# Optimization experiments

Hardware: AMD Instinct MI355X
Metric: run time of the kernel (lower is better)

## Reference

```python
import jax, jax.numpy as jnp
import numpy as np

# ---------- e3nn-style machinery, max_l = 1, real basis ----------
_EPS3 = np.zeros((3, 3, 3), dtype=np.float64)
_EPS3[0, 1, 2] = _EPS3[1, 2, 0] = _EPS3[2, 0, 1] = 1.0
_EPS3[0, 2, 1] = _EPS3[2, 1, 0] = _EPS3[1, 0, 2] = -1.0
W3J = {
    (0, 0, 0): np.ones((1, 1, 1)),
    (0, 1, 1): np.eye(3)[None, :, :] / np.sqrt(3.0),
    (1, 0, 1): np.eye(3)[:, None, :] / np.sqrt(3.0),
    (1, 1, 0): np.eye(3)[:, :, None] / np.sqrt(3.0),
    (1, 1, 1): _EPS3 / np.sqrt(6.0),
}

# irreps as (mul, l, parity)
IR_SH    = [(1, 0, 1), (1, 1, -1)]                      # 1x0e+1x1o (dim 4)
IR_INTER = [(4, 0, 1), (4, 0, -1), (2, 1, -1), (2, 1, 1)]  # gate.irreps_in (dim 20)
IR_GOUT  = [(2, 0, 1), (2, 0, -1), (2, 1, -1), (2, 1, 1)]  # gate.irreps_out (dim 16)
IR_OUT   = [(1, 1, -1), (1, 1, 1)]                      # 1x1o+1x1e (dim 6)

def _offsets(ir):
    off, o = [], 0
    for m, l, _ in ir:
        off.append(o)
        o += m * (2 * l + 1)
    return off, o

def build_tp(ir1, ir2, iro):
    """Fully-connected TP instructions: component irrep-norm, element path-norm."""
    fan = [0.0] * len(iro)
    paths = []
    for io, (mo, lo, po) in enumerate(iro):
        for i1, (m1, l1, p1) in enumerate(ir1):
            for i2, (m2, l2, p2) in enumerate(ir2):
                if p1 * p2 == po and abs(l1 - l2) <= lo <= l1 + l2:
                    paths.append((i1, i2, io))
                    fan[io] += m1 * m2
    ins, woff = [], 0
    for i1, i2, io in paths:
        m1, l1, _ = ir1[i1]; m2, l2, _ = ir2[i2]; mo, lo, _ = iro[io]
        alpha = float(np.sqrt((2 * lo + 1) / fan[io]))
        ins.append((i1, i2, io, alpha, woff))
        woff += m1 * m2 * mo
    return ins, woff

INS1, NUMEL1 = build_tp(IR_SH, IR_SH, IR_INTER)   # weight_numel = 14
INS2, NUMEL2 = build_tp(IR_GOUT, IR_SH, IR_OUT)   # weight_numel = 12

def tp_apply(ir1, ir2, iro, ins, x1, x2, w):
    off1, _ = _offsets(ir1); off2, _ = _offsets(ir2); offo, _ = _offsets(iro)
    lead = x1.shape[:-1]
    out = [None] * len(iro)
    for i1, i2, io, alpha, woff in ins:
        m1, l1, _ = ir1[i1]; m2, l2, _ = ir2[i2]; mo, lo, _ = iro[io]
        x1b = x1[..., off1[i1]:off1[i1] + m1 * (2 * l1 + 1)].reshape(lead + (m1, 2 * l1 + 1))
        x2b = x2[..., off2[i2]:off2[i2] + m2 * (2 * l2 + 1)].reshape(lead + (m2, 2 * l2 + 1))
        wb = w[..., woff:woff + m1 * m2 * mo].reshape(lead + (m1, m2, mo))
        C = jnp.asarray(W3J[(l1, l2, lo)], dtype=x1.dtype)
        blk = alpha * jnp.einsum('...ui,...vj,ijk,...uvw->...wk', x1b, x2b, C, wb)
        out[io] = blk if out[io] is None else out[io] + blk
    pieces = []
    for io, (mo, lo, _) in enumerate(iro):
        b = out[io] if out[io] is not None else jnp.zeros(lead + (mo, 2 * lo + 1), x1.dtype)
        pieces.append(b.reshape(lead + (mo * (2 * lo + 1),)))
    return jnp.concatenate(pieces, axis=-1)

def fc_net(x, w1, w2):
    # e3nn FullyConnectedNet: h = relu(x @ W1 / sqrt(fan_in)) * sqrt(2); out = h @ W2 / sqrt(fan)
    h = jax.nn.relu(x @ w1 / np.sqrt(w1.shape[0])) * np.sqrt(2.0)
    return h @ w2 / np.sqrt(w2.shape[0])

def gate_fn(x):
    # input irreps: [4x0e | 4x0o | 2x1o | 2x1e]; within 0e: 2 scalars + gates g1,g3; within 0o: 2 scalars + gates g2,g4
    lead = x.shape[:-1]
    se = jax.nn.relu(x[..., 0:2])
    ge = x[..., 2:4]
    so = jnp.abs(x[..., 4:6])
    go = x[..., 6:8]
    v1o = x[..., 8:14].reshape(lead + (2, 3))
    v1e = x[..., 14:20].reshape(lead + (2, 3))
    g1 = jax.nn.relu(ge[..., 0:1]); g3 = jax.nn.relu(ge[..., 1:2])
    g2 = jnp.tanh(go[..., 0:1]);    g4 = jnp.tanh(go[..., 1:2])
    v1o_out = jnp.concatenate([v1o[..., 0, :] * g1, v1o[..., 1, :] * g2], axis=-1)
    v1e_out = jnp.concatenate([v1e[..., 0, :] * g3, v1e[..., 1, :] * g4], axis=-1)
    return jnp.concatenate([se, so, v1o_out, v1e_out], axis=-1)  # [..., 16]

def sph_l1(d):
    # spherical harmonics l<=1, normalize=True, normalization='component' (e3nn l=1 order: y,z,x)
    n = jnp.sqrt(jnp.sum(d * d, axis=-1, keepdims=True) + 1e-12)
    u = d / n
    ones = jnp.ones(d.shape[:-1] + (1,), d.dtype)
    return jnp.concatenate([ones, np.sqrt(3.0) * u[..., [1, 2, 0]]], axis=-1)  # [..., 4]

def global_conv(ir1, iro, ins, nf, edge_attr, atten, normalizer, w1, w2):
    w = fc_net(atten, w1, w2)                                   # [B,N,N,numel]
    B, N = nf.shape[0], nf.shape[1]
    nfe = jnp.broadcast_to(nf[:, None, :, :], (B, N, N, nf.shape[-1]))  # node j at edge (i,j)
    ef = tp_apply(ir1, IR_SH, iro, ins, nfe, edge_attr, w)      # [B,N,N,dim_out]
    return jnp.sum(ef, axis=1) / normalizer

def _forward(attn_disp, attn_mask, coordinates, fc1_w1, fc1_w2, fc2_w1, fc2_w2):
    B, H, N, _ = attn_disp.shape
    normalizer = jnp.sqrt(jnp.sum((~jnp.isinf(attn_disp[:, 0])).astype(coordinates.dtype), axis=-1))[..., None]  # [B,N,1]
    ad = jnp.transpose(attn_disp, (0, 2, 3, 1))                 # [B,N,N,H]
    ad = jnp.where(jnp.isinf(ad), jnp.zeros((), ad.dtype), ad)
    # unit displacement (zero on diagonal)
    d = coordinates[:, :, None, :] - coordinates[:, None, :, :]
    d = d / (jnp.sqrt(jnp.sum(d * d, axis=-1, keepdims=True) + 1e-12) + 1e-5)
    edge_features = sph_l1(d)                                   # [B,N,N,4]
    nf = jnp.sum(edge_features, axis=1) / normalizer            # [B,N,4]
    nf = global_conv(IR_SH, IR_INTER, INS1, nf, edge_features, ad, normalizer, fc1_w1, fc1_w2)   # [B,N,20]
    nf = gate_fn(nf)                                            # [B,N,16]
    nf = global_conv(IR_GOUT, IR_OUT, INS2, nf, edge_features, ad, normalizer, fc2_w1, fc2_w2)   # [B,N,6]
    return ad, attn_mask, coordinates, nf, edge_features

def setup_inputs() -> dict:
    key = jax.random.key(0)
    ks = jax.random.split(key, 8)
    B, H, N = 4, 16, 512
    return {
        'attn_disp': jax.random.normal(ks[0], (B, H, N, N), jnp.float32),
        'attn_mask': jax.random.normal(ks[1], (B * H, N, N), jnp.float32),
        'coordinates': jax.random.normal(ks[2], (B, N, 3), jnp.float32),
        'fc1_w1': jax.random.normal(ks[3], (H, 2 * H), jnp.float32),
        'fc1_w2': jax.random.normal(ks[4], (2 * H, NUMEL1), jnp.float32),
        'fc2_w1': jax.random.normal(ks[5], (H, 2 * H), jnp.float32),
        'fc2_w2': jax.random.normal(ks[6], (2 * H, NUMEL2), jnp.float32),
    }

def reference(attn_disp, attn_mask, coordinates, fc1_w1, fc1_w2, fc2_w1, fc2_w2):
    return _forward(attn_disp, attn_mask, coordinates, fc1_w1, fc1_w2, fc2_w1, fc2_w2)
```

## Files before the change

### kernel.cpp

```cpp
#include <hip/hip_runtime.h>
#include <cmath>

#define NN 512

__device__ __forceinline__ int is_inf_f(float x) {
    return (__float_as_uint(x) & 0x7fffffffu) == 0x7f800000u;
}

__device__ __forceinline__ void edge_vec(float ci0, float ci1, float ci2,
                                         float cj0, float cj1, float cj2,
                                         float& e0, float& e1, float& e2) {
    float d0 = ci0 - cj0, d1 = ci1 - cj1, d2 = ci2 - cj2;
    float den = sqrtf(d0*d0 + d1*d1 + d2*d2 + 1e-12f) + 1e-5f;
    float r = 1.0f / den;
    d0 *= r; d1 *= r; d2 *= r;
    float n = sqrtf(d0*d0 + d1*d1 + d2*d2 + 1e-12f);
    float s = 1.7320508075688772f / n;
    e0 = d1 * s;
    e1 = d2 * s;
    e2 = d0 * s;
}

__global__ __launch_bounds__(256) void k_stage(
    const float* __restrict__ disp, const float* __restrict__ mask,
    const float* __restrict__ coords,
    float* __restrict__ ad_out, float* __restrict__ mask_out,
    float* __restrict__ coords_out, float* __restrict__ ef_out,
    float* __restrict__ ws_norm)
{
    const int blk = blockIdx.x;
    const int b = blk >> 9, i = blk & 511;
    const int tid = threadIdx.x;
    const float ci0 = coords[(b*NN+i)*3+0];
    const float ci1 = coords[(b*NN+i)*3+1];
    const float ci2 = coords[(b*NN+i)*3+2];
    int cnt = 0;
    #pragma unroll
    for (int r = 0; r < 2; r++) {
        const int j = r*256 + tid;
        float v[16];
        #pragma unroll
        for (int h = 0; h < 16; h++) {
            float x = disp[((b*16+h)*NN + i)*NN + j];
            int bad = is_inf_f(x);
            if (h == 0) cnt += 1 - bad;
            v[h] = bad ? 0.0f : x;
        }
        float4* dst = (float4*)(ad_out + (size_t)((b*NN+i)*NN + j)*16);
        dst[0] = make_float4(v[0], v[1], v[2], v[3]);
        dst[1] = make_float4(v[4], v[5], v[6], v[7]);
        dst[2] = make_float4(v[8], v[9], v[10], v[11]);
        dst[3] = make_float4(v[12], v[13], v[14], v[15]);
        const float cj0 = coords[(b*NN+j)*3+0];
        const float cj1 = coords[(b*NN+j)*3+1];
        const float cj2 = coords[(b*NN+j)*3+2];
        float e0, e1, e2;
        edge_vec(ci0, ci1, ci2, cj0, cj1, cj2, e0, e1, e2);
        ((float4*)ef_out)[(b*NN+i)*NN + j] = make_float4(1.0f, e0, e1, e2);
    }
    {
        const float4* mi = (const float4*)mask;
        float4* mo = (float4*)mask_out;
        const int mbase = blk * 2048;
        #pragma unroll
        for (int r = 0; r < 8; r++) mo[mbase + r*256 + tid] = mi[mbase + r*256 + tid];
    }
    if (blk == 0) {
        for (int idx = tid; idx < 4*NN*3; idx += 256) coords_out[idx] = coords[idx];
    }
    #pragma unroll
    for (int off = 32; off >= 1; off >>= 1) cnt += __shfl_down(cnt, off);
    __shared__ int sred[4];
    if ((tid & 63) == 0) sred[tid >> 6] = cnt;
    __syncthreads();
    if (tid == 0) ws_norm[blk] = sqrtf((float)(sred[0]+sred[1]+sred[2]+sred[3]));
}

__global__ __launch_bounds__(256) void k_reduce(
    const float* __restrict__ ad, const float* __restrict__ coords,
    const float* __restrict__ wA, const float* __restrict__ wB,
    float* __restrict__ ws)
{
    __shared__ float W0[512], W1[512];
    __shared__ float A[256*17];
    __shared__ float E[256*3];
    __shared__ float sred[12];
    const int blk = blockIdx.x;
    const int b = blk >> 9, j = blk & 511;
    const int tid = threadIdx.x;
    const int i_slot = tid & 31, c_slot = tid >> 5, c0 = c_slot * 4;
    W0[tid] = wA[tid]; W0[tid+256] = wA[tid+256];
    W1[tid] = wB[tid]; W1[tid+256] = wB[tid+256];
    const float cj0 = coords[(b*NN+j)*3+0];
    const float cj1 = coords[(b*NN+j)*3+1];
    const float cj2 = coords[(b*NN+j)*3+2];
    float se0 = 0.f, se1 = 0.f, se2 = 0.f;
    float acc[2][4][4];
    #pragma unroll
    for (int n = 0; n < 2; n++)
        #pragma unroll
        for (int c = 0; c < 4; c++)
            #pragma unroll
            for (int w = 0; w < 4; w++) acc[n][c][w] = 0.f;

    for (int s = 0; s < 2; s++) {
        __syncthreads();
        const int i = s*256 + tid;
        const float4* src = (const float4*)(ad + (size_t)((b*NN+i)*NN + j)*16);
        float4 v0 = src[0], v1 = src[1], v2 = src[2], v3 = src[3];
        const int ab = tid*17;
        A[ab+ 0]=v0.x; A[ab+ 1]=v0.y; A[ab+ 2]=v0.z; A[ab+ 3]=v0.w;
        A[ab+ 4]=v1.x; A[ab+ 5]=v1.y; A[ab+ 6]=v1.z; A[ab+ 7]=v1.w;
        A[ab+ 8]=v2.x; A[ab+ 9]=v2.y; A[ab+10]=v2.z; A[ab+11]=v2.w;
        A[ab+12]=v3.x; A[ab+13]=v3.y; A[ab+14]=v3.z; A[ab+15]=v3.w;
        const float ci0 = coords[(b*NN+i)*3+0];
        const float ci1 = coords[(b*NN+i)*3+1];
        const float ci2 = coords[(b*NN+i)*3+2];
        float e0, e1, e2;
        edge_vec(ci0, ci1, ci2, cj0, cj1, cj2, e0, e1, e2);
        E[tid*3+0]=e0; E[tid*3+1]=e1; E[tid*3+2]=e2;
        se0 += e0; se1 += e1; se2 += e2;
        __syncthreads();
        for (int half = 0; half < 2; half++) {
            float a[4][16], ee[4][3];
            #pragma unroll
            for (int q = 0; q < 4; q++) {
                const int il = i_slot + 32*(half*4+q);
                const int ba = il*17;
                #pragma unroll
                for (int h = 0; h < 16; h++) a[q][h] = A[ba+h];
                ee[q][0]=E[il*3+0]; ee[q][1]=E[il*3+1]; ee[q][2]=E[il*3+2];
            }
            #pragma unroll
            for (int c = 0; c < 4; c++) {
                const int cc = c0 + c;
                #pragma unroll
                for (int net = 0; net < 2; net++) {
                    const float* __restrict__ Wn = net ? W1 : W0;
                    float t[4] = {0.f, 0.f, 0.f, 0.f};
                    #pragma unroll
                    for (int h = 0; h < 16; h++) {
                        const float w = Wn[h*32+cc];
                        #pragma unroll
                        for (int q = 0; q < 4; q++) t[q] = fmaf(a[q][h], w, t[q]);
                    }
                    #pragma unroll
                    for (int q = 0; q < 4; q++) {
                        const float hq = fmaxf(t[q]*0.25f, 0.f) * 1.4142135623730951f;
                        acc[net][c][0] += hq;
                        acc[net][c][1] = fmaf(ee[q][0], hq, acc[net][c][1]);
                        acc[net][c][2] = fmaf(ee[q][1], hq, acc[net][c][2]);
                        acc[net][c][3] = fmaf(ee[q][2], hq, acc[net][c][3]);
                    }
                }
            }
        }
    }
    #pragma unroll
    for (int n = 0; n < 2; n++)
        #pragma unroll
        for (int c = 0; c < 4; c++)
            #pragma unroll
            for (int w = 0; w < 4; w++) {
                float v = acc[n][c][w];
                v += __shfl_xor(v, 1); v += __shfl_xor(v, 2); v += __shfl_xor(v, 4);
                v += __shfl_xor(v, 8); v += __shfl_xor(v, 16);
                acc[n][c][w] = v;
            }
    if (i_slot == 0) {
        float* accg = ws + 2048*4 + (size_t)blk*256;
        #pragma unroll
        for (int n = 0; n < 2; n++)
            #pragma unroll
            for (int w = 0; w < 4; w++)
                #pragma unroll
                for (int c = 0; c < 4; c++)
                    accg[(n*4+w)*32 + c0 + c] = acc[n][c][w];
    }
    #pragma unroll
    for (int off = 1; off < 64; off <<= 1) {
        se0 += __shfl_xor(se0, off);
        se1 += __shfl_xor(se1, off);
        se2 += __shfl_xor(se2, off);
    }
    if ((tid & 63) == 0) {
        const int wv = tid >> 6;
        sred[wv*3+0] = se0; sred[wv*3+1] = se1; sred[wv*3+2] = se2;
    }
    __syncthreads();
    if (tid == 0) {
        float* seg = ws + 2048 + blk*3;
        seg[0] = sred[0]+sred[3]+sred[6]+sred[9];
        seg[1] = sred[1]+sred[4]+sred[7]+sred[10];
        seg[2] = sred[2]+sred[5]+sred[8]+sred[11];
    }
}

__global__ __launch_bounds__(256) void k_final(
    const float* __restrict__ ws,
    const float* __restrict__ w2a,
    const float* __restrict__ w2b,
    float* __restrict__ nf_out)
{
    const int bj = blockIdx.x*256 + threadIdx.x;
    const float inv = 1.0f / ws[bj];
    const float s  = 512.0f * inv;
    const float vv0 = ws[2048 + bj*3 + 0] * inv;
    const float vv1 = ws[2048 + bj*3 + 1] * inv;
    const float vv2 = ws[2048 + bj*3 + 2] * inv;
    const float* acc = ws + 2048*4 + (size_t)bj*256;
    const float ksc = 0.17677669529663687f;
    float S0[14], S1[3][14];
    #pragma unroll
    for (int cc = 0; cc < 14; cc++) { S0[cc]=0.f; S1[0][cc]=0.f; S1[1][cc]=0.f; S1[2][cc]=0.f; }
    for (int c = 0; c < 32; c++) {
        const float p = acc[c], q0 = acc[32+c], q1 = acc[64+c], q2 = acc[96+c];
        #pragma unroll
        for (int cc = 0; cc < 14; cc++) {
            const float w = w2a[c*14+cc];
            S0[cc]    = fmaf(p,  w, S0[cc]);
            S1[0][cc] = fmaf(q0, w, S1[0][cc]);
            S1[1][cc] = fmaf(q1, w, S1[1][cc]);
            S1[2][cc] = fmaf(q2, w, S1[2][cc]);
        }
    }
    #pragma unroll
    for (int cc = 0; cc < 14; cc++) { S0[cc]*=ksc; S1[0][cc]*=ksc; S1[1][cc]*=ksc; S1[2][cc]*=ksc; }
    const float is2 = 0.7071067811865476f;
    const float is3 = 0.5773502691896258f;
    float x0[4];
    #pragma unroll
    for (int k = 0; k < 4; k++)
        x0[k] = inv*is2*( s*S0[k] + is3*(vv0*S1[0][4+k] + vv1*S1[1][4+k] + vv2*S1[2][4+k]) );
    const float vv[3] = {vv0, vv1, vv2};
    float x8[3];
    #pragma unroll
    for (int k = 0; k < 3; k++)
        x8[k] = inv*is2*( s*S1[k][8] + vv[k]*S0[10] );
    const float E12_0=S1[0][12], E12_1=S1[1][12], E12_2=S1[2][12];
    float x14[3];
    x14[0] = inv*is2*(vv1*E12_2 - vv2*E12_1);
    x14[1] = inv*is2*(vv2*E12_0 - vv0*E12_2);
    x14[2] = inv*is2*(vv0*E12_1 - vv1*E12_0);
    const float a0 = fmaxf(x0[0],0.f), a1 = fmaxf(x0[1],0.f);
    const float g1 = fmaxf(x0[2],0.f), g3 = fmaxf(x0[3],0.f);
    const float p0=x8[0]*g1,  p1=x8[1]*g1,  p2=x8[2]*g1;
    const float q0_=x14[0]*g3, q1_=x14[1]*g3, q2_=x14[2]*g3;
    float T0[12], T1[3][12];
    #pragma unroll
    for (int cc = 0; cc < 12; cc++){ T0[cc]=0.f; T1[0][cc]=0.f; T1[1][cc]=0.f; T1[2][cc]=0.f; }
    const float* acc2 = acc + 128;
    for (int c = 0; c < 32; c++) {
        const float p = acc2[c], r0 = acc2[32+c], r1 = acc2[64+c], r2 = acc2[96+c];
        #pragma unroll
        for (int cc = 0; cc < 12; cc++) {
            const float w = w2b[c*12+cc];
            T0[cc]    = fmaf(p,  w, T0[cc]);
            T1[0][cc] = fmaf(r0, w, T1[0][cc]);
            T1[1][cc] = fmaf(r1, w, T1[1][cc]);
            T1[2][cc] = fmaf(r2, w, T1[2][cc]);
        }
    }
    #pragma unroll
    for (int cc = 0; cc < 12; cc++){ T0[cc]*=ksc; T1[0][cc]*=ksc; T1[1][cc]*=ksc; T1[2][cc]*=ksc; }
    const float is6  = 0.4082482904638631f;
    const float is12 = 0.28867513459481287f;
    const float E0[3] = {T1[0][0], T1[1][0], T1[2][0]};
    const float E1[3] = {T1[0][1], T1[1][1], T1[2][1]};
    const float E4[3] = {T1[0][4], T1[1][4], T1[2][4]};
    const float E8[3] = {T1[0][8], T1[1][8], T1[2][8]};
    const float cq0 = q1_*E4[2] - q2_*E4[1];
    const float cq1 = q2_*E4[0] - q0_*E4[2];
    const float cq2 = q0_*E4[1] - q1_*E4[0];
    const float cp0 = p1*E8[2] - p2*E8[1];
    const float cp1 = p2*E8[0] - p0*E8[2];
    const float cp2 = p0*E8[1] - p1*E8[0];
    float o[6];
    o[0] = inv*( is6*(a0*E0[0] + a1*E1[0]) + is6*p0*T0[2] + is12*cq0 );
    o[1] = inv*( is6*(a0*E0[1] + a1*E1[1]) + is6*p1*T0[2] + is12*cq1 );
    o[2] = inv*( is6*(a0*E0[2] + a1*E1[2]) + is6*p2*T0[2] + is12*cq2 );
    o[3] = inv*( is12*cp0 + is6*q0_*T0[10] );
    o[4] = inv*( is12*cp1 + is6*q1_*T0[10] );
    o[5] = inv*( is12*cp2 + is6*q2_*T0[10] );
    #pragma unroll
    for (int k = 0; k < 6; k++) nf_out[bj*6+k] = o[k];
}

extern "C" void kernel_launch(void* const* d_in, const int* in_sizes, int n_in,
                              void* d_out, int out_size, void* d_ws, size_t ws_size,
                              hipStream_t stream) {
    const float* disp   = (const float*)d_in[0];
    const float* mask   = (const float*)d_in[1];
    const float* coords = (const float*)d_in[2];
    const float* fc1w1  = (const float*)d_in[3];
    const float* fc1w2  = (const float*)d_in[4];
    const float* fc2w1  = (const float*)d_in[5];
    const float* fc2w2  = (const float*)d_in[6];
    float* out = (float*)d_out;
    float* ad_out     = out;
    float* mask_out   = out + 16777216;
    float* coords_out = out + 33554432;
    float* nf_out     = coords_out + 6144;
    float* ef_out     = nf_out + 12288;
    float* ws = (float*)d_ws;

    k_stage <<<2048, 256, 0, stream>>>(disp, mask, coords, ad_out, mask_out,
                                       coords_out, ef_out, ws);
    k_reduce<<<2048, 256, 0, stream>>>(ad_out, coords, fc1w1, fc2w1, ws);
    k_final <<<8,    256, 0, stream>>>(ws, fc1w2, fc2w2, nf_out);
}
```

Measured before the change: 372.1 us.

## Write transposed attention copy for coalesced reduction, defer mask copy into final kernel

The staging kernel now also writes a transposed [b,j,i,h] copy of the sanitized attention displacement through shared memory. It puts that copy temporarily in the mask output region, so the reduction kernel reads contiguous per-j rows instead of strided column gathers. The reduction kernel is restructured so each wave handles 16 output channels with weights held in registers and the next tile's loads prefetched, dropping the shared-memory staging and most barriers. The mask and coordinate copies move into extra blocks of the final kernel, after the temporary buffer is consumed. This adds a full extra 64MB write and read of the transposed data in exchange for coalesced access.

```diff
diff --git a/kernel.cpp b/kernel.cpp
--- a/kernel.cpp
+++ b/kernel.cpp
@@ -21,27 +21,29 @@
     e2 = d0 * s;
 }
 
-__global__ __launch_bounds__(256) void k_stage(
-    const float* __restrict__ disp, const float* __restrict__ mask,
-    const float* __restrict__ coords,
-    float* __restrict__ ad_out, float* __restrict__ mask_out,
-    float* __restrict__ coords_out, float* __restrict__ ef_out,
-    float* __restrict__ ws_norm)
+__global__ __launch_bounds__(256) void k_trans(
+    const float* __restrict__ disp, const float* __restrict__ coords,
+    float* __restrict__ ad_out, float* __restrict__ adT_out,
+    float* __restrict__ ef_out, float* __restrict__ ws_norm)
 {
+    __shared__ float L[256 * 20];
     const int blk = blockIdx.x;
-    const int b = blk >> 9, i = blk & 511;
+    const int b   = blk >> 7;
+    const int i0  = (blk & 127) << 2;
     const int tid = threadIdx.x;
+    const int il  = tid >> 6;
+    const int jl  = tid & 63;
+    const int i   = i0 + il;
     const float ci0 = coords[(b*NN+i)*3+0];
     const float ci1 = coords[(b*NN+i)*3+1];
     const float ci2 = coords[(b*NN+i)*3+2];
     int cnt = 0;
-    #pragma unroll
-    for (int r = 0; r < 2; r++) {
-        const int j = r*256 + tid;
+    for (int ch = 0; ch < 8; ch++) {
+        const int j = ch*64 + jl;
         float v[16];
         #pragma unroll
         for (int h = 0; h < 16; h++) {
-            float x = disp[((b*16+h)*NN + i)*NN + j];
+            float x = disp[(size_t)((b*16+h)*NN + i)*NN + j];
             int bad = is_inf_f(x);
             if (h == 0) cnt += 1 - bad;
             v[h] = bad ? 0.0f : x;
@@ -51,148 +53,144 @@
         dst[1] = make_float4(v[4], v[5], v[6], v[7]);
         dst[2] = make_float4(v[8], v[9], v[10], v[11]);
         dst[3] = make_float4(v[12], v[13], v[14], v[15]);
-        const float cj0 = coords[(b*NN+j)*3+0];
-        const float cj1 = coords[(b*NN+j)*3+1];
-        const float cj2 = coords[(b*NN+j)*3+2];
-        float e0, e1, e2;
-        edge_vec(ci0, ci1, ci2, cj0, cj1, cj2, e0, e1, e2);
-        ((float4*)ef_out)[(b*NN+i)*NN + j] = make_float4(1.0f, e0, e1, e2);
-    }
-    {
-        const float4* mi = (const float4*)mask;
-        float4* mo = (float4*)mask_out;
-        const int mbase = blk * 2048;
-        #pragma unroll
-        for (int r = 0; r < 8; r++) mo[mbase + r*256 + tid] = mi[mbase + r*256 + tid];
-    }
-    if (blk == 0) {
-        for (int idx = tid; idx < 4*NN*3; idx += 256) coords_out[idx] = coords[idx];
-    }
-    #pragma unroll
-    for (int off = 32; off >= 1; off >>= 1) cnt += __shfl_down(cnt, off);
-    __shared__ int sred[4];
-    if ((tid & 63) == 0) sred[tid >> 6] = cnt;
-    __syncthreads();
-    if (tid == 0) ws_norm[blk] = sqrtf((float)(sred[0]+sred[1]+sred[2]+sred[3]));
-}
-
-__global__ __launch_bounds__(256) void k_reduce(
-    const float* __restrict__ ad, const float* __restrict__ coords,
+        {
+            const float cj0 = coords[(b*NN+j)*3+0];
+            const float cj1 = coords[(b*NN+j)*3+1];
+            const float cj2 = coords[(b*NN+j)*3+2];
+            float e0, e1, e2;
+            edge_vec(ci0, ci1, ci2, cj0, cj1, cj2, e0, e1, e2);
+            ((float4*)ef_out)[(size_t)(b*NN+i)*NN + j] = make_float4(1.0f, e0, e1, e2);
+        }
+        {
+            float4* Lr = (float4*)(L + tid*20);
+            Lr[0] = make_float4(v[0], v[1], v[2], v[3]);
+            Lr[1] = make_float4(v[4], v[5], v[6], v[7]);
+            Lr[2] = make_float4(v[8], v[9], v[10], v[11]);
+            Lr[3] = make_float4(v[12], v[13], v[14], v[15]);
+        }
+        __syncthreads();
+        #pragma unroll
+        for (int p = 0; p < 4; p++) {
+            const int jj  = (tid >> 4) + p*16;
+            const int f   = tid & 15;
+            const int iw  = f >> 2, w4 = f & 3;
+            const int row = iw*64 + jj;
+            float4 val = *(const float4*)(L + row*20 + w4*4);
+            ((float4*)adT_out)[(size_t)((b*NN + ch*64 + jj)*NN + (i0 + iw))*4 + w4] = val;
+        }
+        __syncthreads();
+    }
+    #pragma unroll
+    for (int off = 32; off >= 1; off >>= 1) cnt += __shfl_xor(cnt, off);
+    if (jl == 0) ws_norm[b*NN + i] = sqrtf((float)cnt);
+}
+
+__global__ __launch_bounds__(256) void k_reduce2(
+    const float* __restrict__ adT, const float* __restrict__ coords,
     const float* __restrict__ wA, const float* __restrict__ wB,
     float* __restrict__ ws)
 {
-    __shared__ float W0[512], W1[512];
-    __shared__ float A[256*17];
-    __shared__ float E[256*3];
-    __shared__ float sred[12];
-    const int blk = blockIdx.x;
-    const int b = blk >> 9, j = blk & 511;
-    const int tid = threadIdx.x;
-    const int i_slot = tid & 31, c_slot = tid >> 5, c0 = c_slot * 4;
-    W0[tid] = wA[tid]; W0[tid+256] = wA[tid+256];
-    W1[tid] = wB[tid]; W1[tid+256] = wB[tid+256];
+    const int blk  = blockIdx.x;
+    const int b    = blk >> 9, j = blk & 511;
+    const int tid  = threadIdx.x;
+    const int lane = tid & 63;
+    const int wv   = tid >> 6;
     const float cj0 = coords[(b*NN+j)*3+0];
     const float cj1 = coords[(b*NN+j)*3+1];
     const float cj2 = coords[(b*NN+j)*3+2];
+    float e0[8], e1[8], e2[8];
     float se0 = 0.f, se1 = 0.f, se2 = 0.f;
-    float acc[2][4][4];
-    #pragma unroll
-    for (int n = 0; n < 2; n++)
-        #pragma unroll
-        for (int c = 0; c < 4; c++)
-            #pragma unroll
-            for (int w = 0; w < 4; w++) acc[n][c][w] = 0.f;
-
-    for (int s = 0; s < 2; s++) {
-        __syncthreads();
-        const int i = s*256 + tid;
-        const float4* src = (const float4*)(ad + (size_t)((b*NN+i)*NN + j)*16);
-        float4 v0 = src[0], v1 = src[1], v2 = src[2], v3 = src[3];
-        const int ab = tid*17;
-        A[ab+ 0]=v0.x; A[ab+ 1]=v0.y; A[ab+ 2]=v0.z; A[ab+ 3]=v0.w;
-        A[ab+ 4]=v1.x; A[ab+ 5]=v1.y; A[ab+ 6]=v1.z; A[ab+ 7]=v1.w;
-        A[ab+ 8]=v2.x; A[ab+ 9]=v2.y; A[ab+10]=v2.z; A[ab+11]=v2.w;
-        A[ab+12]=v3.x; A[ab+13]=v3.y; A[ab+14]=v3.z; A[ab+15]=v3.w;
+    #pragma unroll
+    for (int k = 0; k < 8; k++) {
+        const int i = k*64 + lane;
         const float ci0 = coords[(b*NN+i)*3+0];
         const float ci1 = coords[(b*NN+i)*3+1];
         const float ci2 = coords[(b*NN+i)*3+2];
-        float e0, e1, e2;
-        edge_vec(ci0, ci1, ci2, cj0, cj1, cj2, e0, e1, e2);
-        E[tid*3+0]=e0; E[tid*3+1]=e1; E[tid*3+2]=e2;
-        se0 += e0; se1 += e1; se2 += e2;
-        __syncthreads();
-        for (int half = 0; half < 2; half++) {
-            float a[4][16], ee[4][3];
+        edge_vec(ci0, ci1, ci2, cj0, cj1, cj2, e0[k], e1[k], e2[k]);
+        se0 += e0[k]; se1 += e1[k]; se2 += e2[k];
+    }
+    const float* __restrict__ W = (wv & 2) ? wB : wA;
+    const int cbase = (wv & 1) * 16;
+    const size_t abase = (size_t)((b*NN + j) * NN) * 16;
+    float* accg = ws + 2048*4 + (size_t)blk*256;
+    for (int cb = 0; cb < 4; cb++) {
+        float wt[4][16];
+        #pragma unroll
+        for (int cc = 0; cc < 4; cc++) {
+            const int col = __builtin_amdgcn_readfirstlane(cbase + cb*4 + cc);
             #pragma unroll
-            for (int q = 0; q < 4; q++) {
-                const int il = i_slot + 32*(half*4+q);
-                const int ba = il*17;
-                #pragma unroll
-                for (int h = 0; h < 16; h++) a[q][h] = A[ba+h];
-                ee[q][0]=E[il*3+0]; ee[q][1]=E[il*3+1]; ee[q][2]=E[il*3+2];
+            for (int h = 0; h < 16; h++) wt[cc][h] = W[h*32 + col];
+        }
+        float acc[4][4];
+        #pragma unroll
+        for (int cc = 0; cc < 4; cc++)
+            #pragma unroll
+            for (int w = 0; w < 4; w++) acc[cc][w] = 0.f;
+        float4 A0, A1, A2, A3;
+        {
+            const float4* s = (const float4*)(adT + abase + (size_t)lane*16);
+            A0 = s[0]; A1 = s[1]; A2 = s[2]; A3 = s[3];
+        }
+        #pragma unroll
+        for (int k = 0; k < 8; k++) {
+            float4 N0, N1, N2, N3;
+            if (k < 7) {
+                const float4* s = (const float4*)(adT + abase + (size_t)((k+1)*64 + lane)*16);
+                N0 = s[0]; N1 = s[1]; N2 = s[2]; N3 = s[3];
             }
             #pragma unroll
-            for (int c = 0; c < 4; c++) {
-                const int cc = c0 + c;
-                #pragma unroll
-                for (int net = 0; net < 2; net++) {
-                    const float* __restrict__ Wn = net ? W1 : W0;
-                    float t[4] = {0.f, 0.f, 0.f, 0.f};
-                    #pragma unroll
-                    for (int h = 0; h < 16; h++) {
-                        const float w = Wn[h*32+cc];
-                        #pragma unroll
-                        for (int q = 0; q < 4; q++) t[q] = fmaf(a[q][h], w, t[q]);
-                    }
-                    #pragma unroll
-                    for (int q = 0; q < 4; q++) {
-                        const float hq = fmaxf(t[q]*0.25f, 0.f) * 1.4142135623730951f;
-                        acc[net][c][0] += hq;
-                        acc[net][c][1] = fmaf(ee[q][0], hq, acc[net][c][1]);
-                        acc[net][c][2] = fmaf(ee[q][1], hq, acc[net][c][2]);
-                        acc[net][c][3] = fmaf(ee[q][2], hq, acc[net][c][3]);
-                    }
+            for (int cc = 0; cc < 4; cc++) {
+                float t;
+                t = A0.x * wt[cc][0];
+                t = fmaf(A0.y, wt[cc][1],  t);
+                t = fmaf(A0.z, wt[cc][2],  t);
+                t = fmaf(A0.w, wt[cc][3],  t);
+                t = fmaf(A1.x, wt[cc][4],  t);
+                t = fmaf(A1.y, wt[cc][5],  t);
+                t = fmaf(A1.z, wt[cc][6],  t);
+                t = fmaf(A1.w, wt[cc][7],  t);
+                t = fmaf(A2.x, wt[cc][8],  t);
+                t = fmaf(A2.y, wt[cc][9],  t);
+                t = fmaf(A2.z, wt[cc][10], t);
+                t = fmaf(A2.w, wt[cc][11], t);
+                t = fmaf(A3.x, wt[cc][12], t);
+                t = fmaf(A3.y, wt[cc][13], t);
+                t = fmaf(A3.z, wt[cc][14], t);
+                t = fmaf(A3.w, wt[cc][15], t);
+                const float hq = fmaxf(t * 0.25f, 0.f) * 1.4142135623730951f;
+                acc[cc][0] += hq;
+                acc[cc][1] = fmaf(e0[k], hq, acc[cc][1]);
+                acc[cc][2] = fmaf(e1[k], hq, acc[cc][2]);
+                acc[cc][3] = fmaf(e2[k], hq, acc[cc][3]);
+            }
+            A0 = N0; A1 = N1; A2 = N2; A3 = N3;
+        }
+        #pragma unroll
+        for (int cc = 0; cc < 4; cc++)
+            #pragma unroll
+            for (int w = 0; w < 4; w++) {
+                float vs = acc[cc][w];
+                vs += __shfl_xor(vs, 1);  vs += __shfl_xor(vs, 2);
+                vs += __shfl_xor(vs, 4);  vs += __shfl_xor(vs, 8);
+                vs += __shfl_xor(vs, 16); vs += __shfl_xor(vs, 32);
+                const int q = cc*4 + w;
+                if (lane == q) {
+                    const int C = wv*16 + cb*4 + cc;
+                    accg[((C >> 5)*4 + w)*32 + (C & 31)] = vs;
                 }
             }
-        }
-    }
-    #pragma unroll
-    for (int n = 0; n < 2; n++)
-        #pragma unroll
-        for (int c = 0; c < 4; c++)
-            #pragma unroll
-            for (int w = 0; w < 4; w++) {
-                float v = acc[n][c][w];
-                v += __shfl_xor(v, 1); v += __shfl_xor(v, 2); v += __shfl_xor(v, 4);
-                v += __shfl_xor(v, 8); v += __shfl_xor(v, 16);
-                acc[n][c][w] = v;
-            }
-    if (i_slot == 0) {
-        float* accg = ws + 2048*4 + (size_t)blk*256;
-        #pragma unroll
-        for (int n = 0; n < 2; n++)
-            #pragma unroll
-            for (int w = 0; w < 4; w++)
-                #pragma unroll
-                for (int c = 0; c < 4; c++)
-                    accg[(n*4+w)*32 + c0 + c] = acc[n][c][w];
-    }
-    #pragma unroll
-    for (int off = 1; off < 64; off <<= 1) {
-        se0 += __shfl_xor(se0, off);
-        se1 += __shfl_xor(se1, off);
-        se2 += __shfl_xor(se2, off);
-    }
-    if ((tid & 63) == 0) {
-        const int wv = tid >> 6;
-        sred[wv*3+0] = se0; sred[wv*3+1] = se1; sred[wv*3+2] = se2;
-    }
-    __syncthreads();
-    if (tid == 0) {
-        float* seg = ws + 2048 + blk*3;
-        seg[0] = sred[0]+sred[3]+sred[6]+sred[9];
-        seg[1] = sred[1]+sred[4]+sred[7]+sred[10];
-        seg[2] = sred[2]+sred[5]+sred[8]+sred[11];
+    }
+    if (wv == 0) {
+        #pragma unroll
+        for (int off = 1; off < 64; off <<= 1) {
+            se0 += __shfl_xor(se0, off);
+            se1 += __shfl_xor(se1, off);
+            se2 += __shfl_xor(se2, off);
+        }
+        if (lane == 0) {
+            float* seg = ws + 2048 + blk*3;
+            seg[0] = se0; seg[1] = se1; seg[2] = se2;
+        }
     }
 }
 
@@ -200,8 +198,22 @@
     const float* __restrict__ ws,
     const float* __restrict__ w2a,
     const float* __restrict__ w2b,
-    float* __restrict__ nf_out)
+    float* __restrict__ nf_out,
+    const float* __restrict__ mask, float* __restrict__ mask_out,
+    const float* __restrict__ coords, float* __restrict__ coords_out)
 {
+    if (blockIdx.x >= 8) {
+        const int cblk = blockIdx.x - 8;
+        const float4* mi = (const float4*)mask;
+        float4* mo = (float4*)mask_out;
+        const size_t base = (size_t)cblk * 8192;
+        #pragma unroll
+        for (int r = 0; r < 32; r++) mo[base + r*256 + threadIdx.x] = mi[base + r*256 + threadIdx.x];
+        if (cblk == 0) {
+            for (int idx = threadIdx.x; idx < 4*NN*3; idx += 256) coords_out[idx] = coords[idx];
+        }
+        return;
+    }
     const int bj = blockIdx.x*256 + threadIdx.x;
     const float inv = 1.0f / ws[bj];
     const float s  = 512.0f * inv;
@@ -304,8 +316,10 @@
     float* ef_out     = nf_out + 12288;
     float* ws = (float*)d_ws;
 
-    k_stage <<<2048, 256, 0, stream>>>(disp, mask, coords, ad_out, mask_out,
-                                       coords_out, ef_out, ws);
-    k_reduce<<<2048, 256, 0, stream>>>(ad_out, coords, fc1w1, fc2w1, ws);
-    k_final <<<8,    256, 0, stream>>>(ws, fc1w2, fc2w2, nf_out);
-}
+    float* adT = mask_out;
+
+    k_trans  <<<512,  256, 0, stream>>>(disp, coords, ad_out, adT, ef_out, ws);
+    k_reduce2<<<2048, 256, 0, stream>>>(adT, coords, fc1w1, fc2w1, ws);
+    k_final  <<<520,  256, 0, stream>>>(ws, fc1w2, fc2w2, nf_out,
+                                        mask, mask_out, coords, coords_out);
+}
```

Measured after the change: 414.9 us. 11.5% more time.
